# Optimization experiments

Hardware: AMD Instinct MI355X
Metric: run time of the kernel (lower is better)

The kernel has to match this reference:

```python
import jax, jax.numpy as jnp
import numpy as np

N, D_IN, H, T, O, HOPS = 65536, 128, 64, 12, 3, 4


def setup_inputs() -> dict:
    key = jax.random.key(0)
    ks = jax.random.split(key, 8)
    s = 0.05
    return {
        "x": jax.random.normal(ks[0], (N, D_IN), jnp.float32),
        "proj_W": jax.random.normal(ks[1], (D_IN, H), jnp.float32) * s,
        "proj_b": jnp.zeros((H,), jnp.float32),
        "temper_W1": jax.random.normal(ks[2], (T, O, H, H), jnp.float32) * s,
        "temper_b1": jnp.zeros((T, O, H), jnp.float32),
        "temper_W2": jax.random.normal(ks[3], (T, O, H, H), jnp.float32) * s,
        "temper_b2": jnp.zeros((T, O, H), jnp.float32),
        "route_W1": jax.random.normal(ks[4], (H, H), jnp.float32) * s,
        "route_b1": jnp.zeros((H,), jnp.float32),
        "route_W2": jax.random.normal(ks[5], (H, T + 1), jnp.float32) * s,
        "route_b2": jnp.zeros((T + 1,), jnp.float32),
        "pred_W": jax.random.normal(ks[6], (H, D_IN), jnp.float32) * s,
        "pred_b": jnp.zeros((D_IN,), jnp.float32),
        "init_tempers": jax.random.randint(ks[7], (N,), 0, T),
    }


def reference(x, proj_W, proj_b, temper_W1, temper_b1, temper_W2, temper_b2,
              route_W1, route_b1, route_W2, route_b2, pred_W, pred_b, init_tempers):
    relu = jax.nn.relu
    # input projection; num_patches = hidden // hidden = 1, so tokens == batch rows
    states = x @ proj_W + proj_b                      # [N, H]
    tempers = init_tempers                            # [N] int
    done = jnp.zeros((x.shape[0],), dtype=bool)
    rkey = jax.random.key(42)                         # per-call randomness (mixture weights, sampling)
    for hop in range(HOPS):
        active = ~done
        hkey = jax.random.fold_in(rkey, hop)
        out = jnp.zeros_like(states)
        # dense dispatch: each temper's 3-operator mixture applied, selected per-token by assignment
        for t in range(T):
            w = jax.nn.softmax(jax.random.normal(jax.random.fold_in(hkey, t), (O,)))
            h1 = relu(jnp.einsum('nh,ohk->onk', states, temper_W1[t]) + temper_b1[t][:, None, :])  # [O,N,H]
            h2 = relu(jnp.einsum('onh,ohk->onk', h1, temper_W2[t]) + temper_b2[t][:, None, :])     # [O,N,H]
            out_t = jnp.einsum('o,onk->nk', w, h2)    # mixture over operators
            out = jnp.where((tempers == t)[:, None], out_t, out)
        # routing policy on temper outputs, then multinomial sampling of next temper / STOP
        logits = relu(out @ route_W1 + route_b1) @ route_W2 + route_b2  # [N, T+1]
        sampled = jax.random.categorical(jax.random.fold_in(hkey, 10000), logits)  # [N]
        done_now = sampled == T
        states = jnp.where(active[:, None], out, states)
        tempers = jnp.where(active, jnp.clip(sampled, 0, T - 1).astype(tempers.dtype), tempers)
        done = done | (active & done_now)
    # num_patches == 1 -> mean over patch dim is identity
    pred = states @ pred_W + pred_b                   # [N, D_IN]
    err = jnp.mean((pred - x) ** 2, axis=-1)          # [N]
    return pred, err
```

## Files before the change

kernel.cpp:

```cpp
#include <hip/hip_runtime.h>
#include <cstring>
#include <cmath>
#include <cstdint>

#define N_TOK 65536
#define DIN 128
#define HD 64
#define TN 12
#define ON 3
#define NHOPS 4
#define TPB 256
#define TOKB 64
#define NCAT 13

typedef __attribute__((ext_vector_type(8))) short short8v;
typedef __attribute__((ext_vector_type(4))) float f32x4;
typedef __attribute__((ext_vector_type(4))) unsigned short ushort4v;
typedef __attribute__((ext_vector_type(8))) unsigned short ushort8v;

struct HopConst {
  float w[TN][ON];
  unsigned ck0, ck1;
  int last_hop;
};

__host__ __device__ __forceinline__ void tf2x32(unsigned k0, unsigned k1,
                                                unsigned x0, unsigned x1,
                                                unsigned& o0, unsigned& o1) {
  unsigned ks2 = k0 ^ k1 ^ 0x1BD11BDAu;
  x0 += k0; x1 += k1;
#define TFR(r) { x0 += x1; x1 = (x1 << (r)) | (x1 >> (32 - (r))); x1 ^= x0; }
  TFR(13) TFR(15) TFR(26) TFR(6)
  x0 += k1;  x1 += ks2 + 1u;
  TFR(17) TFR(29) TFR(16) TFR(24)
  x0 += ks2; x1 += k0 + 2u;
  TFR(13) TFR(15) TFR(26) TFR(6)
  x0 += k0;  x1 += k1 + 3u;
  TFR(17) TFR(29) TFR(16) TFR(24)
  x0 += k1;  x1 += ks2 + 4u;
  TFR(13) TFR(15) TFR(26) TFR(6)
  x0 += ks2; x1 += k0 + 5u;
#undef TFR
  o0 = x0; o1 = x1;
}
__host__ __device__ __forceinline__ unsigned tf_bits32(unsigned k0, unsigned k1, unsigned j) {
  unsigned o0, o1;
  tf2x32(k0, k1, 0u, j, o0, o1);
  return o0 ^ o1;
}

__host__ __device__ __forceinline__ unsigned short bf16r(float v) {
  unsigned u = __builtin_bit_cast(unsigned, v);
  return (unsigned short)((u + 0x7fffu + ((u >> 16) & 1u)) >> 16);
}
__host__ __device__ __forceinline__ float bf2f(unsigned short s) {
  return __builtin_bit_cast(float, ((unsigned)s) << 16);
}
__host__ __device__ __forceinline__ void split3(float v, unsigned short& a,
                                                unsigned short& b, unsigned short& c) {
  a = bf16r(v); float r = v - bf2f(a);
  b = bf16r(r); r -= bf2f(b);
  c = bf16r(r);
}


__global__ __launch_bounds__(512, 4) void k_init(
    const float* __restrict__ x, const unsigned short* __restrict__ pjf,
    const float* __restrict__ pb, const int* __restrict__ itemp,
    float* __restrict__ states, int* __restrict__ tempers,
    int* __restrict__ done, int* __restrict__ cnt0)
{
  __shared__ unsigned short sX[3 * 64 * 128];
  __shared__ float sOut[64 * 64];
  __shared__ int lcnt[TN];
  const int tid = threadIdx.x;
  const int lane = tid & 63;
  const int w = __builtin_amdgcn_readfirstlane(tid >> 6);
  const int mgrp = w & 1, ngrp = w >> 1;
  const int bstart = blockIdx.x * 64;

  {
    const int tok = tid >> 3, c0 = tid & 7;
    const float* xr = x + (size_t)(bstart + tok) * DIN + c0 * 16;
    float v[16];
    #pragma unroll
    for (int q = 0; q < 4; ++q) {
      const float4 f = *(const float4*)(xr + q * 4);
      v[q*4] = f.x; v[q*4+1] = f.y; v[q*4+2] = f.z; v[q*4+3] = f.w;
    }
    unsigned short sp[3][16];
    #pragma unroll
    for (int i = 0; i < 16; ++i) split3(v[i], sp[0][i], sp[1][i], sp[2][i]);
    #pragma unroll
    for (int s = 0; s < 3; ++s)
      #pragma unroll
      for (int jj = 0; jj < 2; ++jj) {
        ushort8v u;
        #pragma unroll
        for (int i = 0; i < 8; ++i) u[i] = sp[s][jj * 8 + i];
        const int chunk = (2 * c0 + jj) ^ (tok & 7);
        *(ushort8v*)(sX + s * 8192 + tok * 128 + chunk * 8) = u;
      }
  }
  if (tid < TN) lcnt[tid] = 0;
  __syncthreads();

  const f32x4 zf = {0.0f, 0.0f, 0.0f, 0.0f};
  const int tok16 = (lane & 15) + 16 * ngrp;
  short8v bf[3][4];
  #pragma unroll
  for (int s = 0; s < 3; ++s)
    #pragma unroll
    for (int kc = 0; kc < 4; ++kc) {
      const int chunk = (4 * kc + (lane >> 4)) ^ (tok16 & 7);
      bf[s][kc] = *(const short8v*)(sX + s * 8192 + tok16 * 128 + chunk * 8);
    }
  f32x4 acc[2] = {zf, zf};
  #pragma unroll
  for (int sw = 0; sw < 3; ++sw) {
    short8v a[2][4];
    #pragma unroll
    for (int mt = 0; mt < 2; ++mt)
      #pragma unroll
      for (int kc = 0; kc < 4; ++kc)
        a[mt][kc] = *(const short8v*)(pjf +
            (size_t)((sw * 4 + (2 * mgrp + mt)) * 4 + kc) * 512 + lane * 8);
    #pragma unroll
    for (int sa = 0; sa < 3; ++sa) {
      if (sw + sa > 2) continue;
      #pragma unroll
      for (int mt = 0; mt < 2; ++mt)
        #pragma unroll
        for (int kc = 0; kc < 4; ++kc)
          acc[mt] = __builtin_amdgcn_mfma_f32_16x16x32_bf16(
              a[mt][kc], bf[sa][kc], acc[mt], 0, 0, 0);
    }
  }

  #pragma unroll
  for (int mt = 0; mt < 2; ++mt) {
    const int mt2 = 2 * mgrp + mt;
    const int j0 = 16 * mt2 + 4 * (lane >> 4);
    const float4 bv = *(const float4*)(pb + j0);
    const float bb[4] = {bv.x, bv.y, bv.z, bv.w};
    f32x4 vv;
    #pragma unroll
    for (int r = 0; r < 4; ++r) vv[r] = acc[mt][r] + bb[r];
    const int chunk = (4 * mt2 + (lane >> 4)) ^ (tok16 & 15);
    *(f32x4*)(sOut + tok16 * 64 + chunk * 4) = vv;
  }
  __syncthreads();

  {
    const int tok = tid >> 3, c0 = tid & 7;
    const int n = bstart + tok;
    float* wr = states + (size_t)n * HD;
    #pragma unroll
    for (int q = 0; q < 2; ++q) {
      const int c = c0 + 8 * q;
      const int cs = c ^ (tok & 15);
      *(float4*)(wr + c * 4) = *(const float4*)(sOut + tok * 64 + cs * 4);
    }
  }
  if (tid < 64) {
    const int n = bstart + tid;
    const int t = itemp[n];
    tempers[n] = t;
    done[n] = 0;
    atomicAdd(&lcnt[t], 1);
  }
  __syncthreads();
  if (tid < TN && lcnt[tid] > 0) atomicAdd(&cnt0[tid], lcnt[tid]);
}

__global__ __launch_bounds__(TPB) void k_wprep(
    const float* __restrict__ W1, const float* __restrict__ W2,
    const float* __restrict__ rW1, const float* __restrict__ rW2,
    const float* __restrict__ pjW, const float* __restrict__ pdW,
    unsigned short* __restrict__ w1f, unsigned short* __restrict__ w2f,
    unsigned short* __restrict__ rw1f, unsigned short* __restrict__ rw2f,
    unsigned short* __restrict__ pjf, unsigned short* __restrict__ pwf)
{
  const int idx = blockIdx.x * TPB + threadIdx.x;
  const int NU1 = TN * ON * 4 * 2 * 64;
  const int NU2 = 4 * 2 * 64;
  const int NU3 = 2 * 64;
  const int NU4 = 4 * 4 * 64;
  const int NU5 = 8 * 2 * 64;
  if (idx < NU1) {
    const int lane = idx & 63, kc = (idx >> 6) & 1, mt = (idx >> 7) & 3, mat = idx >> 9;
    const int j = 16 * mt + (lane & 15);
    const int h0 = 32 * kc + 8 * (lane >> 4);
    const float* s1 = W1 + (size_t)mat * 4096;
    const float* s2 = W2 + (size_t)mat * 4096;
    #pragma unroll
    for (int i = 0; i < 8; ++i) {
      unsigned short a0, a1, a2;
      const size_t base = (size_t)mat * 12288 + (size_t)(mt * 2 + kc) * 512 + lane * 8 + i;
      split3(s1[(h0 + i) * 64 + j], a0, a1, a2);
      w1f[base] = a0; w1f[base + 4096] = a1; w1f[base + 8192] = a2;
      split3(s2[(h0 + i) * 64 + j], a0, a1, a2);
      w2f[base] = a0; w2f[base + 4096] = a1; w2f[base + 8192] = a2;
    }
  } else if (idx < NU1 + NU2) {
    const int u = idx - NU1;
    const int lane = u & 63, kc = (u >> 6) & 1, mt = (u >> 7) & 3;
    const int j = 16 * mt + (lane & 15);
    const int h0 = 32 * kc + 8 * (lane >> 4);
    #pragma unroll
    for (int i = 0; i < 8; ++i) {
      unsigned short a0, a1, a2;
      const size_t base = (size_t)(mt * 2 + kc) * 512 + lane * 8 + i;
      split3(rW1[(h0 + i) * 64 + j], a0, a1, a2);
      rw1f[base] = a0; rw1f[base + 4096] = a1; rw1f[base + 8192] = a2;
    }
  } else if (idx < NU1 + NU2 + NU3) {
    const int u = idx - NU1 - NU2;
    const int lane = u & 63, kc = (u >> 6) & 1;
    const int c = lane & 15;
    const int h0 = 32 * kc + 8 * (lane >> 4);
    #pragma unroll
    for (int i = 0; i < 8; ++i) {
      unsigned short a0, a1, a2;
      const float v = (c < NCAT) ? rW2[(h0 + i) * NCAT + c] : 0.0f;
      split3(v, a0, a1, a2);
      const size_t base = (size_t)kc * 512 + lane * 8 + i;
      rw2f[base] = a0; rw2f[base + 1024] = a1; rw2f[base + 2048] = a2;
    }
  } else if (idx < NU1 + NU2 + NU3 + NU4) {
    const int u = idx - (NU1 + NU2 + NU3);
    const int lane = u & 63, kc = (u >> 6) & 3, mt = u >> 8;
    const int j = 16 * mt + (lane & 15);
    const int k0 = 32 * kc + 8 * (lane >> 4);
    #pragma unroll
    for (int i = 0; i < 8; ++i) {
      unsigned short a0, a1, a2;
      split3(pjW[(size_t)(k0 + i) * 64 + j], a0, a1, a2);
      const size_t base = (size_t)(mt * 4 + kc) * 512 + lane * 8 + i;
      pjf[base] = a0; pjf[base + 8192] = a1; pjf[base + 16384] = a2;
    }
  } else if (idx < NU1 + NU2 + NU3 + NU4 + NU5) {
    const int u = idx - (NU1 + NU2 + NU3 + NU4);
    const int lane = u & 63, kc = (u >> 6) & 1, mt = u >> 7;
    const int d = 16 * mt + (lane & 15);
    const int h0 = 32 * kc + 8 * (lane >> 4);
    #pragma unroll
    for (int i = 0; i < 8; ++i) {
      unsigned short a0, a1, a2;
      split3(pdW[(size_t)(h0 + i) * 128 + d], a0, a1, a2);
      const size_t base = (size_t)(mt * 2 + kc) * 512 + lane * 8 + i;
      pwf[base] = a0; pwf[base + 8192] = a1; pwf[base + 16384] = a2;
    }
  }
}

__global__ void k_prefix(const int* __restrict__ cnt, int* __restrict__ offp) {
  if (threadIdx.x == 0 && blockIdx.x == 0) {
    int o = 0;
    for (int t = 0; t < TN; ++t) { offp[t] = o; o += (cnt[t] + TOKB - 1) & ~(TOKB - 1); }
    offp[TN] = o;
  }
}

__global__ __launch_bounds__(TPB) void k_scatter(
    const int* __restrict__ tempers, const int* __restrict__ done,
    const int* __restrict__ offp, int* __restrict__ cursor, int* __restrict__ compact)
{
  __shared__ int lcnt[TN], lbase[TN];
  const int tid = threadIdx.x;
  if (tid < TN) lcnt[tid] = 0;
  __syncthreads();
  const int n = blockIdx.x * TPB + tid;
  int t = -1, lpos = 0;
  if (!done[n]) { t = tempers[n]; lpos = atomicAdd(&lcnt[t], 1); }
  __syncthreads();
  if (tid < TN && lcnt[tid] > 0) lbase[tid] = atomicAdd(&cursor[tid], lcnt[tid]);
  __syncthreads();
  if (t >= 0) compact[offp[t] + lbase[t] + lpos] = n;
}


__device__ __forceinline__ void load_bf(const unsigned short* src, int lane, short8v bf[3][2]) {
  const int n = lane & 15, g = lane >> 4;
  #pragma unroll
  for (int s = 0; s < 3; ++s)
    #pragma unroll
    for (int kc = 0; kc < 2; ++kc) {
      const int chunk = (4 * kc + g) ^ (n & 7);
      bf[s][kc] = *(const short8v*)(src + s * 1024 + n * 64 + chunk * 8);
    }
}

__device__ __forceinline__ void mfma_all4(const unsigned short* __restrict__ Ag,
                                          const short8v bf[3][2], int lane, f32x4 acc[4]) {
  #pragma unroll
  for (int sw = 0; sw < 3; ++sw) {
    short8v a[4][2];
    #pragma unroll
    for (int mt = 0; mt < 4; ++mt)
      #pragma unroll
      for (int kc = 0; kc < 2; ++kc)
        a[mt][kc] = *(const short8v*)(Ag +
            (size_t)((sw * 4 + mt) * 2 + kc) * 512 + lane * 8);
    #pragma unroll
    for (int sa = 0; sa < 3; ++sa) {
      if (sw + sa > 2) continue;
      #pragma unroll
      for (int mt = 0; mt < 4; ++mt)
        #pragma unroll
        for (int kc = 0; kc < 2; ++kc)
          acc[mt] = __builtin_amdgcn_mfma_f32_16x16x32_bf16(
              a[mt][kc], bf[sa][kc], acc[mt], 0, 0, 0);
    }
  }
}

__device__ __forceinline__ void store4_rb(const f32x4 acc[4], const float* __restrict__ bias,
                                          unsigned short* dst, int lane) {
  const int n = lane & 15, g = lane >> 4;
  #pragma unroll
  for (int mt = 0; mt < 4; ++mt) {
    const int j0 = 16 * mt + 4 * g;
    const float4 bv = *(const float4*)(bias + j0);
    const float bb[4] = {bv.x, bv.y, bv.z, bv.w};
    ushort4v u0, u1, u2;
    #pragma unroll
    for (int r = 0; r < 4; ++r) {
      const float v = fmaxf(acc[mt][r] + bb[r], 0.0f);
      unsigned short a, b, c;
      split3(v, a, b, c);
      u0[r] = a; u1[r] = b; u2[r] = c;
    }
    const int idx = n * 64 + ((2 * mt + (g >> 1)) ^ (n & 7)) * 8 + 4 * (g & 1);
    *(ushort4v*)(dst + idx) = u0;
    *(ushort4v*)(dst + 1024 + idx) = u1;
    *(ushort4v*)(dst + 2048 + idx) = u2;
  }
}

__device__ __forceinline__ void store4_raw(const f32x4 acc[4], unsigned short* dst, int lane) {
  const int n = lane & 15, g = lane >> 4;
  #pragma unroll
  for (int mt = 0; mt < 4; ++mt) {
    ushort4v u0, u1, u2;
    #pragma unroll
    for (int r = 0; r < 4; ++r) {
      unsigned short a, b, c;
      split3(acc[mt][r], a, b, c);
      u0[r] = a; u1[r] = b; u2[r] = c;
    }
    const int idx = n * 64 + ((2 * mt + (g >> 1)) ^ (n & 7)) * 8 + 4 * (g & 1);
    *(ushort4v*)(dst + idx) = u0;
    *(ushort4v*)(dst + 1024 + idx) = u1;
    *(ushort4v*)(dst + 2048 + idx) = u2;
  }
}

__global__ __launch_bounds__(TPB, 4) void k_hop(
    float* __restrict__ states, int* __restrict__ tempers, int* __restrict__ done,
    const int* __restrict__ compact, const int* __restrict__ cnt,
    const int* __restrict__ offp,
    const unsigned short* __restrict__ w1f, const float* __restrict__ b1,
    const unsigned short* __restrict__ w2f, const float* __restrict__ b2,
    const unsigned short* __restrict__ rw1f, const float* __restrict__ rb1,
    const unsigned short* __restrict__ rw2f, const float* __restrict__ rb2,
    int* __restrict__ cnt_next, HopConst hc)
{
  __shared__ unsigned short scr[4][3072];
  __shared__ int lcnt[TN];

  const int tid = threadIdx.x;
  const int lane = tid & 63;
  const int wid = __builtin_amdgcn_readfirstlane(tid >> 6);
  unsigned short* ws = scr[wid];
  const int bstart = blockIdx.x * TOKB;
  if (bstart >= offp[TN]) return;
  if (tid < TN) lcnt[tid] = 0;
  int tt = 0;
  #pragma unroll
  for (int i = 1; i < TN; ++i) if (bstart >= offp[i]) tt = i;
  const int t = __builtin_amdgcn_readfirstlane(tt);
  const int cntt = cnt[t];
  const int n = lane & 15, g = lane >> 4;
  const int pos = bstart + wid * 16 + n;
  const bool act = (pos - offp[t]) < cntt;
  const int tok = compact[act ? pos : offp[t]];

  short8v bx[3][2];
  {
    const float* sr = states + (size_t)tok * HD;
    float va[8], vb[8];
    #pragma unroll
    for (int q = 0; q < 2; ++q) {
      const float4 f0 = *(const float4*)(sr + 8 * g + q * 4);
      const float4 f1 = *(const float4*)(sr + 32 + 8 * g + q * 4);
      va[q*4] = f0.x; va[q*4+1] = f0.y; va[q*4+2] = f0.z; va[q*4+3] = f0.w;
      vb[q*4] = f1.x; vb[q*4+1] = f1.y; vb[q*4+2] = f1.z; vb[q*4+3] = f1.w;
    }
    unsigned short sa_[3][8], sb_[3][8];
    #pragma unroll
    for (int i = 0; i < 8; ++i) {
      split3(va[i], sa_[0][i], sa_[1][i], sa_[2][i]);
      split3(vb[i], sb_[0][i], sb_[1][i], sb_[2][i]);
    }
    #pragma unroll
    for (int s = 0; s < 3; ++s) {
      short8v u0, u1;
      #pragma unroll
      for (int i = 0; i < 8; ++i) { u0[i] = (short)sa_[s][i]; u1[i] = (short)sb_[s][i]; }
      bx[s][0] = u0; bx[s][1] = u1;
    }
  }
  __syncthreads();

  const f32x4 zf = {0.0f, 0.0f, 0.0f, 0.0f};
  f32x4 out4[4] = {zf, zf, zf, zf};

  #pragma unroll 1
  for (int o = 0; o < ON; ++o) {
    const int mat = t * ON + o;
    f32x4 acc[4] = {zf, zf, zf, zf};
    mfma_all4(w1f + (size_t)mat * 12288, bx, lane, acc);
    store4_rb(acc, b1 + mat * 64, ws, lane);
    short8v bh[3][2];
    load_bf(ws, lane, bh);
    f32x4 acc2[4] = {zf, zf, zf, zf};
    mfma_all4(w2f + (size_t)mat * 12288, bh, lane, acc2);
    const float wo = hc.w[t][o];
    #pragma unroll
    for (int mt = 0; mt < 4; ++mt) {
      const float4 bv = *(const float4*)(b2 + mat * 64 + 16 * mt + 4 * g);
      const float bb[4] = {bv.x, bv.y, bv.z, bv.w};
      #pragma unroll
      for (int r = 0; r < 4; ++r)
        out4[mt][r] = fmaf(wo, fmaxf(acc2[mt][r] + bb[r], 0.0f), out4[mt][r]);
    }
  }

  if (act) {
    float* wr = states + (size_t)tok * HD;
    #pragma unroll
    for (int mt = 0; mt < 4; ++mt) {
      float4 v; v.x = out4[mt][0]; v.y = out4[mt][1]; v.z = out4[mt][2]; v.w = out4[mt][3];
      *(float4*)(wr + 16 * mt + 4 * g) = v;
    }
  }

  if (!hc.last_hop) {
    store4_raw(out4, ws, lane);
    short8v bo[3][2];
    load_bf(ws, lane, bo);
    f32x4 accr[4] = {zf, zf, zf, zf};
    mfma_all4(rw1f, bo, lane, accr);
    store4_rb(accr, rb1, ws, lane);
    short8v br[3][2];
    load_bf(ws, lane, br);

    f32x4 lg = zf;
    #pragma unroll
    for (int sw = 0; sw < 3; ++sw) {
      short8v a2[2];
      #pragma unroll
      for (int kc = 0; kc < 2; ++kc)
        a2[kc] = *(const short8v*)(rw2f + (size_t)(sw * 2 + kc) * 512 + lane * 8);
      #pragma unroll
      for (int sa = 0; sa < 3; ++sa) {
        if (sw + sa > 2) continue;
        #pragma unroll
        for (int kc = 0; kc < 2; ++kc)
          lg = __builtin_amdgcn_mfma_f32_16x16x32_bf16(a2[kc], br[sa][kc], lg, 0, 0, 0);
      }
    }

    float best = -3.0e38f; int bc = 0;
    const unsigned jbase = (unsigned)tok * (unsigned)NCAT;
    #pragma unroll
    for (int r = 0; r < 4; ++r) {
      const int c = 4 * g + r;
      if (c < NCAT) {
        const unsigned bits = tf_bits32(hc.ck0, hc.ck1, jbase + (unsigned)c);
        const float u = __uint_as_float((bits >> 9) | 0x3f800000u) - 1.0f;
        float val = u + 1.17549435e-38f;
        val = fmaxf(val, 1.17549435e-38f);
        const float gum = -logf(-logf(val));
        const float sc = lg[r] + rb2[c] + gum;
        if (sc > best) { best = sc; bc = c; }
      }
    }
    #pragma unroll
    for (int off = 16; off <= 32; off <<= 1) {
      const float ob = __shfl_xor(best, off, 64);
      const int oc = __shfl_xor(bc, off, 64);
      if (ob > best || (ob == best && oc < bc)) { best = ob; bc = oc; }
    }
    if (g == 0 && act) {
      const int nt = bc < (TN - 1) ? bc : (TN - 1);
      tempers[tok] = nt;
      if (bc == TN) done[tok] = 1;
      else atomicAdd(&lcnt[nt], 1);
    }
    __syncthreads();
    if (tid < TN && lcnt[tid] > 0) atomicAdd(&cnt_next[tid], lcnt[tid]);
  }
}

__global__ __launch_bounds__(512, 4) void k_pred(
    const float* __restrict__ states, const float* __restrict__ x,
    const unsigned short* __restrict__ pwf, const float* __restrict__ pdb,
    float* __restrict__ pred, float* __restrict__ err)
{
  __shared__ unsigned short sX[3 * 64 * 64];
  __shared__ float sP[64 * 128];
  const int tid = threadIdx.x;
  const int lane = tid & 63;
  const int w = __builtin_amdgcn_readfirstlane(tid >> 6);
  const int mgrp = w & 3, ngrp = w >> 2;
  const int bstart = blockIdx.x * 64;

  {
    const int tok = tid >> 3, c0 = tid & 7;
    const float* sr = states + (size_t)(bstart + tok) * HD + c0 * 8;
    float v[8];
    #pragma unroll
    for (int q = 0; q < 2; ++q) {
      const float4 f = *(const float4*)(sr + q * 4);
      v[q*4] = f.x; v[q*4+1] = f.y; v[q*4+2] = f.z; v[q*4+3] = f.w;
    }
    unsigned short sp[3][8];
    #pragma unroll
    for (int i = 0; i < 8; ++i) split3(v[i], sp[0][i], sp[1][i], sp[2][i]);
    const int chunk = c0 ^ (tok & 7);
    #pragma unroll
    for (int s = 0; s < 3; ++s) {
      ushort8v u;
      #pragma unroll
      for (int i = 0; i < 8; ++i) u[i] = sp[s][i];
      *(ushort8v*)(sX + s * 4096 + tok * 64 + chunk * 8) = u;
    }
  }
  __syncthreads();

  const f32x4 zf = {0.0f, 0.0f, 0.0f, 0.0f};
  short8v bf[3][2][2];
  #pragma unroll
  for (int s = 0; s < 3; ++s)
    #pragma unroll
    for (int nt = 0; nt < 2; ++nt)
      #pragma unroll
      for (int kc = 0; kc < 2; ++kc) {
        const int tk = (lane & 15) + 16 * (2 * ngrp + nt);
        const int chunk = (4 * kc + (lane >> 4)) ^ (tk & 7);
        bf[s][nt][kc] = *(const short8v*)(sX + s * 4096 + tk * 64 + chunk * 8);
      }

  f32x4 acc[2][2] = {{zf, zf}, {zf, zf}};
  #pragma unroll
  for (int sw = 0; sw < 3; ++sw) {
    short8v a[2][2];
    #pragma unroll
    for (int mt = 0; mt < 2; ++mt)
      #pragma unroll
      for (int kc = 0; kc < 2; ++kc)
        a[mt][kc] = *(const short8v*)(pwf +
            (size_t)((sw * 8 + (2 * mgrp + mt)) * 2 + kc) * 512 + lane * 8);
    #pragma unroll
    for (int sa = 0; sa < 3; ++sa) {
      if (sw + sa > 2) continue;
      #pragma unroll
      for (int mt = 0; mt < 2; ++mt)
        #pragma unroll
        for (int nt = 0; nt < 2; ++nt)
          #pragma unroll
          for (int kc = 0; kc < 2; ++kc)
            acc[mt][nt] = __builtin_amdgcn_mfma_f32_16x16x32_bf16(
                a[mt][kc], bf[sa][nt][kc], acc[mt][nt], 0, 0, 0);
    }
  }

  #pragma unroll
  for (int mt = 0; mt < 2; ++mt) {
    const int mt2 = 2 * mgrp + mt;
    const int d0 = 16 * mt2 + 4 * (lane >> 4);
    const float4 bv = *(const float4*)(pdb + d0);
    const float bb[4] = {bv.x, bv.y, bv.z, bv.w};
    #pragma unroll
    for (int nt = 0; nt < 2; ++nt) {
      const int tok = (lane & 15) + 16 * (2 * ngrp + nt);
      f32x4 vv;
      #pragma unroll
      for (int r = 0; r < 4; ++r) vv[r] = acc[mt][nt][r] + bb[r];
      const int chunk = (d0 >> 2) ^ (tok & 7);
      *(f32x4*)(sP + tok * 128 + chunk * 4) = vv;
    }
  }
  __syncthreads();

  {
    const int tok = tid >> 3, c0 = tid & 7;
    const int n = bstart + tok;
    const float* xr = x + (size_t)n * DIN;
    float* pr = pred + (size_t)n * DIN;
    float s = 0.0f;
    #pragma unroll
    for (int q = 0; q < 4; ++q) {
      const int c = c0 + 8 * q;
      const int cs = c ^ (tok & 7);
      const f32x4 pv = *(const f32x4*)(sP + tok * 128 + cs * 4);
      const float4 xv = *(const float4*)(xr + c * 4);
      float4 ov; ov.x = pv[0]; ov.y = pv[1]; ov.z = pv[2]; ov.w = pv[3];
      *(float4*)(pr + c * 4) = ov;
      const float e0 = pv[0] - xv.x, e1 = pv[1] - xv.y, e2 = pv[2] - xv.z, e3 = pv[3] - xv.w;
      s += e0 * e0 + e1 * e1 + e2 * e2 + e3 * e3;
    }
    s += __shfl_xor(s, 1, 64);
    s += __shfl_xor(s, 2, 64);
    s += __shfl_xor(s, 4, 64);
    if (c0 == 0) err[n] = s * (1.0f / 128.0f);
  }
}

static float host_erfinv(float xf) {
  double x = xf;
  double w = -log1p(-x * x);
  double p;
  if (w < 5.0) {
    w -= 2.5;
    p = 2.81022636e-08;          p = 3.43273939e-07 + p * w;
    p = -3.5233877e-06 + p * w;  p = -4.39150654e-06 + p * w;
    p = 0.00021858087 + p * w;   p = -0.00125372503 + p * w;
    p = -0.00417768164 + p * w;  p = 0.246640727 + p * w;
    p = 1.50140941 + p * w;
  } else {
    w = sqrt(w) - 3.0;
    p = -0.000200214257;         p = 0.000100950558 + p * w;
    p = 0.00134934322 + p * w;   p = -0.00367342844 + p * w;
    p = 0.00573950773 + p * w;   p = -0.0076224613 + p * w;
    p = 0.00943887047 + p * w;   p = 1.00167406 + p * w;
    p = 2.83297682 + p * w;
  }
  return (float)(p * x);
}

static void build_hops(HopConst* hcs) {
  const float lo = nextafterf(-1.0f, 0.0f);
  const unsigned rk0 = 0u, rk1 = 42u;
  for (int hop = 0; hop < NHOPS; ++hop) {
    unsigned hk0, hk1;
    tf2x32(rk0, rk1, 0u, (unsigned)hop, hk0, hk1);
    for (int t = 0; t < TN; ++t) {
      unsigned tk0, tk1;
      tf2x32(hk0, hk1, 0u, (unsigned)t, tk0, tk1);
      double nrm[3];
      for (int i = 0; i < 3; ++i) {
        const unsigned bits = tf_bits32(tk0, tk1, (unsigned)i);
        unsigned ub = (bits >> 9) | 0x3f800000u;
        float f; memcpy(&f, &ub, 4);
        const float u01 = f - 1.0f;
        float val = u01 * 2.0f + lo;
        if (val < lo) val = lo;
        const float ef = host_erfinv(val);
        nrm[i] = (double)(1.41421356f * ef);
      }
      const double m = fmax(nrm[0], fmax(nrm[1], nrm[2]));
      const double e0 = exp(nrm[0] - m), e1 = exp(nrm[1] - m), e2 = exp(nrm[2] - m);
      const double s = e0 + e1 + e2;
      hcs[hop].w[t][0] = (float)(e0 / s);
      hcs[hop].w[t][1] = (float)(e1 / s);
      hcs[hop].w[t][2] = (float)(e2 / s);
    }
    unsigned ck0, ck1;
    tf2x32(hk0, hk1, 0u, 10000u, ck0, ck1);
    hcs[hop].ck0 = ck0; hcs[hop].ck1 = ck1;
    hcs[hop].last_hop = (hop == NHOPS - 1) ? 1 : 0;
  }
}

extern "C" void kernel_launch(void* const* d_in, const int* in_sizes, int n_in,
                              void* d_out, int out_size, void* d_ws, size_t ws_size,
                              hipStream_t stream) {
  (void)in_sizes; (void)n_in; (void)out_size; (void)ws_size;
  const float* x    = (const float*)d_in[0];
  const float* pW   = (const float*)d_in[1];
  const float* pb   = (const float*)d_in[2];
  const float* W1   = (const float*)d_in[3];
  const float* b1   = (const float*)d_in[4];
  const float* W2   = (const float*)d_in[5];
  const float* b2   = (const float*)d_in[6];
  const float* rW1  = (const float*)d_in[7];
  const float* rb1  = (const float*)d_in[8];
  const float* rW2  = (const float*)d_in[9];
  const float* rb2  = (const float*)d_in[10];
  const float* pdW  = (const float*)d_in[11];
  const float* pdb  = (const float*)d_in[12];
  const int*   itmp = (const int*)d_in[13];

  int* meta    = (int*)d_ws;
  int* tempers = (int*)((char*)d_ws + 1024);
  int* done    = tempers + N_TOK;
  int* compact = done + N_TOK;
  float* states = (float*)(compact + N_TOK + TN * TOKB);
  unsigned short* w1f  = (unsigned short*)(states + (size_t)N_TOK * HD);
  unsigned short* w2f  = w1f + (size_t)TN * ON * 12288;
  unsigned short* rw1f = w2f + (size_t)TN * ON * 12288;
  unsigned short* rw2f = rw1f + 12288;
  unsigned short* pjf  = rw2f + 3072;
  unsigned short* pwf  = pjf + 24576;

  HopConst hcs[NHOPS];
  build_hops(hcs);

  hipMemsetAsync(meta, 0, 160 * sizeof(int), stream);
  k_wprep<<<83, TPB, 0, stream>>>(W1, W2, rW1, rW2, pW, pdW,
                                  w1f, w2f, rw1f, rw2f, pjf, pwf);
  k_init<<<N_TOK / 64, 512, 0, stream>>>(x, pjf, pb, itmp, states, tempers, done, meta);
  for (int h = 0; h < NHOPS; ++h) {
    int* cnt_h = meta + h * TN;
    int* cnt_n = meta + (h + 1) * TN;
    int* cur_h = meta + 60 + h * TN;
    int* off_h = meta + 108 + h * (TN + 1);
    k_prefix<<<1, 64, 0, stream>>>(cnt_h, off_h);
    k_scatter<<<N_TOK / TPB, TPB, 0, stream>>>(tempers, done, off_h, cur_h, compact);
    k_hop<<<N_TOK / TOKB + TN, TPB, 0, stream>>>(states, tempers, done, compact, cnt_h, off_h,
        w1f, b1, w2f, b2, rw1f, rb1, rw2f, rb2, cnt_n, hcs[h]);
  }
  float* pred = (float*)d_out;
  float* errp = pred + (size_t)N_TOK * DIN;
  k_pred<<<N_TOK / 64, 512, 0, stream>>>(states, x, pwf, pdb, pred, errp);
}
```

Before: 236.8 us.

## Process two 16-token tiles per wave to reuse weight fragments in hop kernel

Each wave in the hop kernel now handles 32 tokens (two N-tiles) instead of 16, so every weight A-fragment loaded from global memory feeds two MFMAs. The block size in tokens doubles to 128, LDS scratch per wave doubles, and launch bounds drop to 2 blocks per SM to allow the larger register footprint. This cuts weight-load traffic per token, at the cost of higher register pressure, lower occupancy, and more padding waste at temper-segment boundaries.

```diff
diff --git a/kernel.cpp b/kernel.cpp
--- a/kernel.cpp
+++ b/kernel.cpp
@@ -10,7 +10,7 @@
 #define ON 3
 #define NHOPS 4
 #define TPB 256
-#define TOKB 64
+#define TOKB 128
 #define NCAT 13
 
 typedef __attribute__((ext_vector_type(8))) short short8v;
@@ -280,19 +280,23 @@
 }
 
 
-__device__ __forceinline__ void load_bf(const unsigned short* src, int lane, short8v bf[3][2]) {
+__device__ __forceinline__ void load_bf2(const unsigned short* src, int lane,
+                                         short8v bf[3][2][2]) {
   const int n = lane & 15, g = lane >> 4;
   #pragma unroll
   for (int s = 0; s < 3; ++s)
     #pragma unroll
-    for (int kc = 0; kc < 2; ++kc) {
-      const int chunk = (4 * kc + g) ^ (n & 7);
-      bf[s][kc] = *(const short8v*)(src + s * 1024 + n * 64 + chunk * 8);
-    }
-}
-
-__device__ __forceinline__ void mfma_all4(const unsigned short* __restrict__ Ag,
-                                          const short8v bf[3][2], int lane, f32x4 acc[4]) {
+    for (int nt = 0; nt < 2; ++nt)
+      #pragma unroll
+      for (int kc = 0; kc < 2; ++kc) {
+        const int chunk = (4 * kc + g) ^ (n & 7);
+        bf[s][nt][kc] = *(const short8v*)(src + s * 2048 + (n + 16 * nt) * 64 + chunk * 8);
+      }
+}
+
+__device__ __forceinline__ void mfma_allB(const unsigned short* __restrict__ Ag,
+                                          const short8v bf[3][2][2], int lane,
+                                          f32x4 acc[4][2]) {
   #pragma unroll
   for (int sw = 0; sw < 3; ++sw) {
     short8v a[4][2];
@@ -308,55 +312,61 @@
       #pragma unroll
       for (int mt = 0; mt < 4; ++mt)
         #pragma unroll
-        for (int kc = 0; kc < 2; ++kc)
-          acc[mt] = __builtin_amdgcn_mfma_f32_16x16x32_bf16(
-              a[mt][kc], bf[sa][kc], acc[mt], 0, 0, 0);
-    }
-  }
-}
-
-__device__ __forceinline__ void store4_rb(const f32x4 acc[4], const float* __restrict__ bias,
+        for (int nt = 0; nt < 2; ++nt)
+          #pragma unroll
+          for (int kc = 0; kc < 2; ++kc)
+            acc[mt][nt] = __builtin_amdgcn_mfma_f32_16x16x32_bf16(
+                a[mt][kc], bf[sa][nt][kc], acc[mt][nt], 0, 0, 0);
+    }
+  }
+}
+
+__device__ __forceinline__ void store8_rb(const f32x4 acc[4][2], const float* __restrict__ bias,
                                           unsigned short* dst, int lane) {
   const int n = lane & 15, g = lane >> 4;
   #pragma unroll
   for (int mt = 0; mt < 4; ++mt) {
-    const int j0 = 16 * mt + 4 * g;
-    const float4 bv = *(const float4*)(bias + j0);
+    const float4 bv = *(const float4*)(bias + 16 * mt + 4 * g);
     const float bb[4] = {bv.x, bv.y, bv.z, bv.w};
-    ushort4v u0, u1, u2;
-    #pragma unroll
-    for (int r = 0; r < 4; ++r) {
-      const float v = fmaxf(acc[mt][r] + bb[r], 0.0f);
-      unsigned short a, b, c;
-      split3(v, a, b, c);
-      u0[r] = a; u1[r] = b; u2[r] = c;
-    }
-    const int idx = n * 64 + ((2 * mt + (g >> 1)) ^ (n & 7)) * 8 + 4 * (g & 1);
-    *(ushort4v*)(dst + idx) = u0;
-    *(ushort4v*)(dst + 1024 + idx) = u1;
-    *(ushort4v*)(dst + 2048 + idx) = u2;
-  }
-}
-
-__device__ __forceinline__ void store4_raw(const f32x4 acc[4], unsigned short* dst, int lane) {
+    #pragma unroll
+    for (int nt = 0; nt < 2; ++nt) {
+      ushort4v u0, u1, u2;
+      #pragma unroll
+      for (int r = 0; r < 4; ++r) {
+        const float v = fmaxf(acc[mt][nt][r] + bb[r], 0.0f);
+        unsigned short a, b, c;
+        split3(v, a, b, c);
+        u0[r] = a; u1[r] = b; u2[r] = c;
+      }
+      const int idx = (n + 16 * nt) * 64 + ((2 * mt + (g >> 1)) ^ (n & 7)) * 8 + 4 * (g & 1);
+      *(ushort4v*)(dst + idx) = u0;
+      *(ushort4v*)(dst + 2048 + idx) = u1;
+      *(ushort4v*)(dst + 4096 + idx) = u2;
+    }
+  }
+}
+
+__device__ __forceinline__ void store8_raw(const f32x4 acc[4][2], unsigned short* dst, int lane) {
   const int n = lane & 15, g = lane >> 4;
   #pragma unroll
-  for (int mt = 0; mt < 4; ++mt) {
-    ushort4v u0, u1, u2;
-    #pragma unroll
-    for (int r = 0; r < 4; ++r) {
-      unsigned short a, b, c;
-      split3(acc[mt][r], a, b, c);
-      u0[r] = a; u1[r] = b; u2[r] = c;
-    }
-    const int idx = n * 64 + ((2 * mt + (g >> 1)) ^ (n & 7)) * 8 + 4 * (g & 1);
-    *(ushort4v*)(dst + idx) = u0;
-    *(ushort4v*)(dst + 1024 + idx) = u1;
-    *(ushort4v*)(dst + 2048 + idx) = u2;
-  }
-}
-
-__global__ __launch_bounds__(TPB, 4) void k_hop(
+  for (int mt = 0; mt < 4; ++mt)
+    #pragma unroll
+    for (int nt = 0; nt < 2; ++nt) {
+      ushort4v u0, u1, u2;
+      #pragma unroll
+      for (int r = 0; r < 4; ++r) {
+        unsigned short a, b, c;
+        split3(acc[mt][nt][r], a, b, c);
+        u0[r] = a; u1[r] = b; u2[r] = c;
+      }
+      const int idx = (n + 16 * nt) * 64 + ((2 * mt + (g >> 1)) ^ (n & 7)) * 8 + 4 * (g & 1);
+      *(ushort4v*)(dst + idx) = u0;
+      *(ushort4v*)(dst + 2048 + idx) = u1;
+      *(ushort4v*)(dst + 4096 + idx) = u2;
+    }
+}
+
+__global__ __launch_bounds__(TPB, 2) void k_hop(
     float* __restrict__ states, int* __restrict__ tempers, int* __restrict__ done,
     const int* __restrict__ compact, const int* __restrict__ cnt,
     const int* __restrict__ offp,
@@ -366,7 +376,7 @@
     const unsigned short* __restrict__ rw2f, const float* __restrict__ rb2,
     int* __restrict__ cnt_next, HopConst hc)
 {
-  __shared__ unsigned short scr[4][3072];
+  __shared__ unsigned short scr[4][6144];
   __shared__ int lcnt[TN];
 
   const int tid = threadIdx.x;
@@ -382,13 +392,19 @@
   const int t = __builtin_amdgcn_readfirstlane(tt);
   const int cntt = cnt[t];
   const int n = lane & 15, g = lane >> 4;
-  const int pos = bstart + wid * 16 + n;
-  const bool act = (pos - offp[t]) < cntt;
-  const int tok = compact[act ? pos : offp[t]];
-
-  short8v bx[3][2];
-  {
-    const float* sr = states + (size_t)tok * HD;
+
+  int tok[2]; bool act[2];
+  #pragma unroll
+  for (int nt = 0; nt < 2; ++nt) {
+    const int pos = bstart + wid * 32 + nt * 16 + n;
+    act[nt] = (pos - offp[t]) < cntt;
+    tok[nt] = compact[act[nt] ? pos : offp[t]];
+  }
+
+  short8v bx[3][2][2];
+  #pragma unroll
+  for (int nt = 0; nt < 2; ++nt) {
+    const float* sr = states + (size_t)tok[nt] * HD;
     float va[8], vb[8];
     #pragma unroll
     for (int q = 0; q < 2; ++q) {
@@ -408,55 +424,61 @@
       short8v u0, u1;
       #pragma unroll
       for (int i = 0; i < 8; ++i) { u0[i] = (short)sa_[s][i]; u1[i] = (short)sb_[s][i]; }
-      bx[s][0] = u0; bx[s][1] = u1;
+      bx[s][nt][0] = u0; bx[s][nt][1] = u1;
     }
   }
   __syncthreads();
 
   const f32x4 zf = {0.0f, 0.0f, 0.0f, 0.0f};
-  f32x4 out4[4] = {zf, zf, zf, zf};
+  f32x4 out8[4][2] = {{zf, zf}, {zf, zf}, {zf, zf}, {zf, zf}};
 
   #pragma unroll 1
   for (int o = 0; o < ON; ++o) {
     const int mat = t * ON + o;
-    f32x4 acc[4] = {zf, zf, zf, zf};
-    mfma_all4(w1f + (size_t)mat * 12288, bx, lane, acc);
-    store4_rb(acc, b1 + mat * 64, ws, lane);
-    short8v bh[3][2];
-    load_bf(ws, lane, bh);
-    f32x4 acc2[4] = {zf, zf, zf, zf};
-    mfma_all4(w2f + (size_t)mat * 12288, bh, lane, acc2);
+    f32x4 acc[4][2] = {{zf, zf}, {zf, zf}, {zf, zf}, {zf, zf}};
+    mfma_allB(w1f + (size_t)mat * 12288, bx, lane, acc);
+    store8_rb(acc, b1 + mat * 64, ws, lane);
+    short8v bh[3][2][2];
+    load_bf2(ws, lane, bh);
+    f32x4 acc2[4][2] = {{zf, zf}, {zf, zf}, {zf, zf}, {zf, zf}};
+    mfma_allB(w2f + (size_t)mat * 12288, bh, lane, acc2);
     const float wo = hc.w[t][o];
     #pragma unroll
     for (int mt = 0; mt < 4; ++mt) {
       const float4 bv = *(const float4*)(b2 + mat * 64 + 16 * mt + 4 * g);
       const float bb[4] = {bv.x, bv.y, bv.z, bv.w};
       #pragma unroll
-      for (int r = 0; r < 4; ++r)
-        out4[mt][r] = fmaf(wo, fmaxf(acc2[mt][r] + bb[r], 0.0f), out4[mt][r]);
-    }
-  }
-
-  if (act) {
-    float* wr = states + (size_t)tok * HD;
-    #pragma unroll
-    for (int mt = 0; mt < 4; ++mt) {
-      float4 v; v.x = out4[mt][0]; v.y = out4[mt][1]; v.z = out4[mt][2]; v.w = out4[mt][3];
-      *(float4*)(wr + 16 * mt + 4 * g) = v;
+      for (int nt = 0; nt < 2; ++nt)
+        #pragma unroll
+        for (int r = 0; r < 4; ++r)
+          out8[mt][nt][r] = fmaf(wo, fmaxf(acc2[mt][nt][r] + bb[r], 0.0f), out8[mt][nt][r]);
+    }
+  }
+
+  #pragma unroll
+  for (int nt = 0; nt < 2; ++nt) {
+    if (act[nt]) {
+      float* wr = states + (size_t)tok[nt] * HD;
+      #pragma unroll
+      for (int mt = 0; mt < 4; ++mt) {
+        float4 v; v.x = out8[mt][nt][0]; v.y = out8[mt][nt][1];
+        v.z = out8[mt][nt][2]; v.w = out8[mt][nt][3];
+        *(float4*)(wr + 16 * mt + 4 * g) = v;
+      }
     }
   }
 
   if (!hc.last_hop) {
-    store4_raw(out4, ws, lane);
-    short8v bo[3][2];
-    load_bf(ws, lane, bo);
-    f32x4 accr[4] = {zf, zf, zf, zf};
-    mfma_all4(rw1f, bo, lane, accr);
-    store4_rb(accr, rb1, ws, lane);
-    short8v br[3][2];
-    load_bf(ws, lane, br);
-
-    f32x4 lg = zf;
+    store8_raw(out8, ws, lane);
+    short8v bo[3][2][2];
+    load_bf2(ws, lane, bo);
+    f32x4 accr[4][2] = {{zf, zf}, {zf, zf}, {zf, zf}, {zf, zf}};
+    mfma_allB(rw1f, bo, lane, accr);
+    store8_rb(accr, rb1, ws, lane);
+    short8v br[3][2][2];
+    load_bf2(ws, lane, br);
+
+    f32x4 lg[2] = {zf, zf};
     #pragma unroll
     for (int sw = 0; sw < 3; ++sw) {
       short8v a2[2];
@@ -467,37 +489,43 @@
       for (int sa = 0; sa < 3; ++sa) {
         if (sw + sa > 2) continue;
         #pragma unroll
-        for (int kc = 0; kc < 2; ++kc)
-          lg = __builtin_amdgcn_mfma_f32_16x16x32_bf16(a2[kc], br[sa][kc], lg, 0, 0, 0);
-      }
-    }
-
-    float best = -3.0e38f; int bc = 0;
-    const unsigned jbase = (unsigned)tok * (unsigned)NCAT;
-    #pragma unroll
-    for (int r = 0; r < 4; ++r) {
-      const int c = 4 * g + r;
-      if (c < NCAT) {
-        const unsigned bits = tf_bits32(hc.ck0, hc.ck1, jbase + (unsigned)c);
-        const float u = __uint_as_float((bits >> 9) | 0x3f800000u) - 1.0f;
-        float val = u + 1.17549435e-38f;
-        val = fmaxf(val, 1.17549435e-38f);
-        const float gum = -logf(-logf(val));
-        const float sc = lg[r] + rb2[c] + gum;
-        if (sc > best) { best = sc; bc = c; }
-      }
-    }
-    #pragma unroll
-    for (int off = 16; off <= 32; off <<= 1) {
-      const float ob = __shfl_xor(best, off, 64);
-      const int oc = __shfl_xor(bc, off, 64);
-      if (ob > best || (ob == best && oc < bc)) { best = ob; bc = oc; }
-    }
-    if (g == 0 && act) {
-      const int nt = bc < (TN - 1) ? bc : (TN - 1);
-      tempers[tok] = nt;
-      if (bc == TN) done[tok] = 1;
-      else atomicAdd(&lcnt[nt], 1);
+        for (int nt = 0; nt < 2; ++nt)
+          #pragma unroll
+          for (int kc = 0; kc < 2; ++kc)
+            lg[nt] = __builtin_amdgcn_mfma_f32_16x16x32_bf16(a2[kc], br[sa][nt][kc],
+                                                             lg[nt], 0, 0, 0);
+      }
+    }
+
+    #pragma unroll
+    for (int nt = 0; nt < 2; ++nt) {
+      float best = -3.0e38f; int bc = 0;
+      const unsigned jbase = (unsigned)tok[nt] * (unsigned)NCAT;
+      #pragma unroll
+      for (int r = 0; r < 4; ++r) {
+        const int c = 4 * g + r;
+        if (c < NCAT) {
+          const unsigned bits = tf_bits32(hc.ck0, hc.ck1, jbase + (unsigned)c);
+          const float u = __uint_as_float((bits >> 9) | 0x3f800000u) - 1.0f;
+          float val = u + 1.17549435e-38f;
+          val = fmaxf(val, 1.17549435e-38f);
+          const float gum = -logf(-logf(val));
+          const float sc = lg[nt][r] + rb2[c] + gum;
+          if (sc > best) { best = sc; bc = c; }
+        }
+      }
+      #pragma unroll
+      for (int off = 16; off <= 32; off <<= 1) {
+        const float ob = __shfl_xor(best, off, 64);
+        const int oc = __shfl_xor(bc, off, 64);
+        if (ob > best || (ob == best && oc < bc)) { best = ob; bc = oc; }
+      }
+      if (g == 0 && act[nt]) {
+        const int ntp = bc < (TN - 1) ? bc : (TN - 1);
+        tempers[tok[nt]] = ntp;
+        if (bc == TN) done[tok[nt]] = 1;
+        else atomicAdd(&lcnt[ntp], 1);
+      }
     }
     __syncthreads();
     if (tid < TN && lcnt[tid] > 0) atomicAdd(&cnt_next[tid], lcnt[tid]);
```

Result: slower. 268.2 us (+13.3%).

## Use packed bf16 conversion for 3-way split and hoist all weight loads

Applied to the files above, without the earlier changes.

Replaces the software round-to-nearest bf16 three-way split with the hardware v_cvt_pk_bf16_f32 instruction, which converts two floats per instruction. This is applied in the hidden-state stores and in the token input conversion. All 24 weight fragments are now loaded before the MFMA loop rather than per split, giving the loads more time to arrive. Launch bounds are relaxed from 4 to 2 waves per SIMD, which lets the kernel use more registers for the hoisted fragments at the cost of occupancy.

```diff
diff --git a/kernel.cpp b/kernel.cpp
--- a/kernel.cpp
+++ b/kernel.cpp
@@ -17,6 +17,8 @@
 typedef __attribute__((ext_vector_type(4))) float f32x4;
 typedef __attribute__((ext_vector_type(4))) unsigned short ushort4v;
 typedef __attribute__((ext_vector_type(8))) unsigned short ushort8v;
+typedef __attribute__((ext_vector_type(2))) unsigned int uint2v;
+typedef __attribute__((ext_vector_type(4))) unsigned int uint4v;
 
 struct HopConst {
   float w[TN][ON];
@@ -61,6 +63,21 @@
   a = bf16r(v); float r = v - bf2f(a);
   b = bf16r(r); r -= bf2f(b);
   c = bf16r(r);
+}
+
+__device__ __forceinline__ void cvtpk3(float v0, float v1,
+                                       unsigned& q0, unsigned& q1, unsigned& q2) {
+  unsigned p0, p1, p2;
+  asm("v_cvt_pk_bf16_f32 %0, %1, %2" : "=v"(p0) : "v"(v0), "v"(v1));
+  const float a0 = __builtin_bit_cast(float, p0 << 16);
+  const float a1 = __builtin_bit_cast(float, p0 & 0xffff0000u);
+  const float r0 = v0 - a0, r1 = v1 - a1;
+  asm("v_cvt_pk_bf16_f32 %0, %1, %2" : "=v"(p1) : "v"(r0), "v"(r1));
+  const float b0 = __builtin_bit_cast(float, p1 << 16);
+  const float b1 = __builtin_bit_cast(float, p1 & 0xffff0000u);
+  const float s0 = r0 - b0, s1 = r1 - b1;
+  asm("v_cvt_pk_bf16_f32 %0, %1, %2" : "=v"(p2) : "v"(s0), "v"(s1));
+  q0 = p0; q1 = p1; q2 = p2;
 }
 
 
@@ -293,15 +310,12 @@
 
 __device__ __forceinline__ void mfma_all4(const unsigned short* __restrict__ Ag,
                                           const short8v bf[3][2], int lane, f32x4 acc[4]) {
-  #pragma unroll
-  for (int sw = 0; sw < 3; ++sw) {
-    short8v a[4][2];
-    #pragma unroll
-    for (int mt = 0; mt < 4; ++mt)
-      #pragma unroll
-      for (int kc = 0; kc < 2; ++kc)
-        a[mt][kc] = *(const short8v*)(Ag +
-            (size_t)((sw * 4 + mt) * 2 + kc) * 512 + lane * 8);
+  short8v a[24];
+  #pragma unroll
+  for (int u = 0; u < 24; ++u)
+    a[u] = *(const short8v*)(Ag + (size_t)u * 512 + lane * 8);
+  #pragma unroll
+  for (int sw = 0; sw < 3; ++sw)
     #pragma unroll
     for (int sa = 0; sa < 3; ++sa) {
       if (sw + sa > 2) continue;
@@ -310,9 +324,8 @@
         #pragma unroll
         for (int kc = 0; kc < 2; ++kc)
           acc[mt] = __builtin_amdgcn_mfma_f32_16x16x32_bf16(
-              a[mt][kc], bf[sa][kc], acc[mt], 0, 0, 0);
-    }
-  }
+              a[sw * 8 + mt * 2 + kc], bf[sa][kc], acc[mt], 0, 0, 0);
+    }
 }
 
 __device__ __forceinline__ void store4_rb(const f32x4 acc[4], const float* __restrict__ bias,
@@ -322,19 +335,17 @@
   for (int mt = 0; mt < 4; ++mt) {
     const int j0 = 16 * mt + 4 * g;
     const float4 bv = *(const float4*)(bias + j0);
-    const float bb[4] = {bv.x, bv.y, bv.z, bv.w};
-    ushort4v u0, u1, u2;
-    #pragma unroll
-    for (int r = 0; r < 4; ++r) {
-      const float v = fmaxf(acc[mt][r] + bb[r], 0.0f);
-      unsigned short a, b, c;
-      split3(v, a, b, c);
-      u0[r] = a; u1[r] = b; u2[r] = c;
-    }
+    const float v0 = fmaxf(acc[mt][0] + bv.x, 0.0f);
+    const float v1 = fmaxf(acc[mt][1] + bv.y, 0.0f);
+    const float v2 = fmaxf(acc[mt][2] + bv.z, 0.0f);
+    const float v3 = fmaxf(acc[mt][3] + bv.w, 0.0f);
+    unsigned q00, q01, q02, q10, q11, q12;
+    cvtpk3(v0, v1, q00, q01, q02);
+    cvtpk3(v2, v3, q10, q11, q12);
     const int idx = n * 64 + ((2 * mt + (g >> 1)) ^ (n & 7)) * 8 + 4 * (g & 1);
-    *(ushort4v*)(dst + idx) = u0;
-    *(ushort4v*)(dst + 1024 + idx) = u1;
-    *(ushort4v*)(dst + 2048 + idx) = u2;
+    *(uint2v*)(dst + idx)        = uint2v{q00, q10};
+    *(uint2v*)(dst + 1024 + idx) = uint2v{q01, q11};
+    *(uint2v*)(dst + 2048 + idx) = uint2v{q02, q12};
   }
 }
 
@@ -342,21 +353,17 @@
   const int n = lane & 15, g = lane >> 4;
   #pragma unroll
   for (int mt = 0; mt < 4; ++mt) {
-    ushort4v u0, u1, u2;
-    #pragma unroll
-    for (int r = 0; r < 4; ++r) {
-      unsigned short a, b, c;
-      split3(acc[mt][r], a, b, c);
-      u0[r] = a; u1[r] = b; u2[r] = c;
-    }
+    unsigned q00, q01, q02, q10, q11, q12;
+    cvtpk3(acc[mt][0], acc[mt][1], q00, q01, q02);
+    cvtpk3(acc[mt][2], acc[mt][3], q10, q11, q12);
     const int idx = n * 64 + ((2 * mt + (g >> 1)) ^ (n & 7)) * 8 + 4 * (g & 1);
-    *(ushort4v*)(dst + idx) = u0;
-    *(ushort4v*)(dst + 1024 + idx) = u1;
-    *(ushort4v*)(dst + 2048 + idx) = u2;
-  }
-}
-
-__global__ __launch_bounds__(TPB, 4) void k_hop(
+    *(uint2v*)(dst + idx)        = uint2v{q00, q10};
+    *(uint2v*)(dst + 1024 + idx) = uint2v{q01, q11};
+    *(uint2v*)(dst + 2048 + idx) = uint2v{q02, q12};
+  }
+}
+
+__global__ __launch_bounds__(TPB, 2) void k_hop(
     float* __restrict__ states, int* __restrict__ tempers, int* __restrict__ done,
     const int* __restrict__ compact, const int* __restrict__ cnt,
     const int* __restrict__ offp,
@@ -397,18 +404,19 @@
       va[q*4] = f0.x; va[q*4+1] = f0.y; va[q*4+2] = f0.z; va[q*4+3] = f0.w;
       vb[q*4] = f1.x; vb[q*4+1] = f1.y; vb[q*4+2] = f1.z; vb[q*4+3] = f1.w;
     }
-    unsigned short sa_[3][8], sb_[3][8];
-    #pragma unroll
-    for (int i = 0; i < 8; ++i) {
-      split3(va[i], sa_[0][i], sa_[1][i], sa_[2][i]);
-      split3(vb[i], sb_[0][i], sb_[1][i], sb_[2][i]);
+    uint4v wa[3], wb[3];
+    #pragma unroll
+    for (int i = 0; i < 4; ++i) {
+      unsigned pa0, pa1, pa2, pb0, pb1, pb2;
+      cvtpk3(va[2*i], va[2*i+1], pa0, pa1, pa2);
+      cvtpk3(vb[2*i], vb[2*i+1], pb0, pb1, pb2);
+      wa[0][i] = pa0; wa[1][i] = pa1; wa[2][i] = pa2;
+      wb[0][i] = pb0; wb[1][i] = pb1; wb[2][i] = pb2;
     }
     #pragma unroll
     for (int s = 0; s < 3; ++s) {
-      short8v u0, u1;
-      #pragma unroll
-      for (int i = 0; i < 8; ++i) { u0[i] = (short)sa_[s][i]; u1[i] = (short)sb_[s][i]; }
-      bx[s][0] = u0; bx[s][1] = u1;
+      bx[s][0] = __builtin_bit_cast(short8v, wa[s]);
+      bx[s][1] = __builtin_bit_cast(short8v, wb[s]);
     }
   }
   __syncthreads();
```

After: 230.6 us. -2.6%, faster.
